# Performance work log

Measured on AMD Instinct MI355X. Metric: run time of the kernel, lower is better.

Reference implementation:

```python
import jax, jax.numpy as jnp
import numpy as np

N_NODES = 100000
N_EDGES = 1600000
G_DIM, H1, H2 = 128, 64, 32
HEADS = 4
NUM_REL = 3
NUM_CLASSES = 7


def setup_inputs() -> dict:
    key = jax.random.key(0)
    ks = jax.random.split(key, 16)
    s = 0.05
    inp = {
        "x": jax.random.normal(ks[0], (N_NODES, G_DIM), dtype=jnp.float32),
        "lengths": N_NODES,
        "edge_index": jax.random.randint(ks[1], (2, N_EDGES), 0, N_NODES),
        "edge_type": jax.random.randint(ks[2], (N_EDGES,), 0, NUM_REL),
        # RGCNConv params (root weight + per-relation weights + bias)
        "W_rel": jax.random.normal(ks[3], (NUM_REL, G_DIM, H1), dtype=jnp.float32) * s,
        "W_root": jax.random.normal(ks[4], (G_DIM, H1), dtype=jnp.float32) * s,
        "b_rgcn": jax.random.normal(ks[5], (H1,), dtype=jnp.float32) * s,
        # TransformerConv params (heads*H2 = 128 output, concat=True default)
        "Wq": jax.random.normal(ks[6], (H1, HEADS * H2), dtype=jnp.float32) * s,
        "bq": jax.random.normal(ks[7], (HEADS * H2,), dtype=jnp.float32) * s,
        "Wk": jax.random.normal(ks[8], (H1, HEADS * H2), dtype=jnp.float32) * s,
        "bk": jax.random.normal(ks[9], (HEADS * H2,), dtype=jnp.float32) * s,
        "Wv": jax.random.normal(ks[10], (H1, HEADS * H2), dtype=jnp.float32) * s,
        "bv": jax.random.normal(ks[11], (HEADS * H2,), dtype=jnp.float32) * s,
        "Wskip": jax.random.normal(ks[12], (H1, HEADS * H2), dtype=jnp.float32) * s,
        "bskip": jax.random.normal(ks[13], (HEADS * H2,), dtype=jnp.float32) * s,
        # final classifier (in = heads*H2 since TransformerConv concat=True)
        "Wf": jax.random.normal(ks[14], (HEADS * H2, NUM_CLASSES), dtype=jnp.float32) * s,
        "bf": jax.random.normal(ks[15], (NUM_CLASSES,), dtype=jnp.float32) * s,
    }
    return inp


def _forward(x, edge_index, edge_type, W_rel, W_root, b_rgcn,
             Wq, bq, Wk, bk, Wv, bv, Wskip, bskip, Wf, bf):
    n = x.shape[0]
    src, dst = edge_index[0], edge_index[1]  # source -> target flow

    # ---- RGCNConv: root transform + per-relation mean aggregation ----
    h = x @ W_root + b_rgcn  # [N, H1]
    for r in range(NUM_REL):
        hr = x @ W_rel[r]  # [N, H1] transform at node level (cheap)
        mask = (edge_type == r)
        msg = jnp.where(mask[:, None], hr[src], 0.0)  # [E, H1]
        ssum = jax.ops.segment_sum(msg, dst, num_segments=n)
        cnt = jax.ops.segment_sum(mask.astype(x.dtype), dst, num_segments=n)
        h = h + jnp.where(cnt[:, None] > 0, ssum / jnp.maximum(cnt, 1.0)[:, None], 0.0)
    h = jax.nn.relu(h)

    # ---- TransformerConv (heads=4, concat=True, root skip) ----
    Q = (h @ Wq + bq).reshape(n, HEADS, H2)
    K = (h @ Wk + bk).reshape(n, HEADS, H2)
    V = (h @ Wv + bv).reshape(n, HEADS, H2)
    scores = jnp.sum(Q[dst] * K[src], axis=-1) / jnp.sqrt(jnp.asarray(H2, x.dtype))  # [E, HEADS]
    smax = jax.ops.segment_max(scores, dst, num_segments=n)  # [N, HEADS]
    e = jnp.exp(scores - smax[dst])
    denom = jax.ops.segment_sum(e, dst, num_segments=n)  # [N, HEADS]
    alpha = e / jnp.maximum(denom[dst], 1e-16)  # [E, HEADS]
    agg = jax.ops.segment_sum(alpha[..., None] * V[src], dst, num_segments=n)  # [N, HEADS, H2]
    out = agg.reshape(n, HEADS * H2) + h @ Wskip + bskip
    out = jax.nn.relu(out)

    return out @ Wf + bf  # [N, NUM_CLASSES]


def reference(x, lengths, edge_index, edge_type, W_rel, W_root, b_rgcn,
              Wq, bq, Wk, bk, Wv, bv, Wskip, bskip, Wf, bf):
    # lengths is accepted but unused by the original forward
    return _forward(x, edge_index, edge_type, W_rel, W_root, b_rgcn,
                    Wq, bq, Wk, bk, Wv, bv, Wskip, bskip, Wf, bf)
```

## Files before the change

kernel.cpp:

```cpp
#include <hip/hip_runtime.h>
#include <math.h>

#define N_NODES 100000
#define N_EDGES 1600000

typedef short short8 __attribute__((ext_vector_type(8)));
typedef float f32x4 __attribute__((ext_vector_type(4)));
typedef float f32x2 __attribute__((ext_vector_type(2)));
typedef _Float16 h2 __attribute__((ext_vector_type(2)));

#define QSC 0.25503540f

static __device__ __forceinline__ float bf2f(unsigned int u16) {
    return __uint_as_float(u16 << 16);
}
static __device__ __forceinline__ unsigned short f2bf(float f) {
    unsigned u = __float_as_uint(f);
    unsigned r = u + 0x7FFF + ((u >> 16) & 1);
    return (unsigned short)(r >> 16);
}
static __device__ __forceinline__ f32x2 bfpair(unsigned u) {
    f32x2 r;
    r.x = __uint_as_float(u << 16);
    r.y = __uint_as_float(u & 0xFFFF0000u);
    return r;
}
static __device__ __forceinline__ float dot8h(const h2* q, uint4 k) {
    h2 s = q[0] * __builtin_bit_cast(h2, k.x);
    s += q[1] * __builtin_bit_cast(h2, k.y);
    s += q[2] * __builtin_bit_cast(h2, k.z);
    s += q[3] * __builtin_bit_cast(h2, k.w);
    return (float)s.x + (float)s.y;
}
static __device__ __forceinline__ void pv8h(h2* o, float w, uint4 v) {
    _Float16 wh = (_Float16)w;
    o[0] += wh * __builtin_bit_cast(h2, v.x);
    o[1] += wh * __builtin_bit_cast(h2, v.y);
    o[2] += wh * __builtin_bit_cast(h2, v.z);
    o[3] += wh * __builtin_bit_cast(h2, v.w);
}

__global__ void repack_kernel(const float* __restrict__ Wrel, const float* __restrict__ Wroot,
                              const float* __restrict__ Wq, const float* __restrict__ Wk,
                              const float* __restrict__ Wv, const float* __restrict__ Wsk,
                              const float* __restrict__ bq, const float* __restrict__ bk,
                              const float* __restrict__ bv, const float* __restrict__ bsk,
                              unsigned short* __restrict__ W1t, unsigned short* __restrict__ W2t,
                              float* __restrict__ bcat) {
    int idx = blockIdx.x * 256 + threadIdx.x;
    if (idx < 128 * 256) {
        int k = idx >> 8, c = idx & 255;
        float v;
        if (c < 192) { int r = c >> 6, cc = c & 63; v = Wrel[r * 8192 + k * 64 + cc]; }
        else v = Wroot[k * 64 + (c - 192)];
        W1t[c * 128 + k] = f2bf(v);
    }
    int i2 = idx - 128 * 256;
    if (i2 >= 0 && i2 < 64 * 512) {
        int k = i2 >> 9, c = i2 & 511;
        float v;
        if (c < 128) v = Wq[k * 128 + c];
        else if (c < 256) v = Wk[k * 128 + c - 128];
        else if (c < 384) v = Wv[k * 128 + c - 256];
        else v = Wsk[k * 128 + c - 384];
        W2t[c * 64 + k] = f2bf(v);
    }
    int i3 = idx - 128 * 256 - 64 * 512;
    if (i3 >= 0 && i3 < 512) {
        float v;
        if (i3 < 128) v = bq[i3];
        else if (i3 < 256) v = bk[i3 - 128];
        else if (i3 < 384) v = bv[i3 - 256];
        else v = bsk[i3 - 384];
        bcat[i3] = v;
    }
}

__global__ void hist_kernel(const int* __restrict__ ei, const int* __restrict__ et,
                            int* __restrict__ cntr) {
    int e = blockIdx.x * 256 + threadIdx.x;
    if (e < N_EDGES) atomicAdd(&cntr[et[e] * N_NODES + ei[N_EDGES + e]], 1);
}

__global__ void scanA_kernel(const int* __restrict__ cntr, int* __restrict__ part) {
    __shared__ int wsum[4];
    int t = threadIdx.x;
    int base = blockIdx.x * 1024 + t * 4;
    int s = 0;
    for (int i = 0; i < 4; i++) {
        int idx = base + i;
        if (idx < N_NODES) s += cntr[idx] + cntr[N_NODES + idx] + cntr[2 * N_NODES + idx];
    }
    for (int off = 1; off < 64; off <<= 1) s += __shfl_xor(s, off);
    if ((t & 63) == 0) wsum[t >> 6] = s;
    __syncthreads();
    if (t == 0) part[blockIdx.x] = wsum[0] + wsum[1] + wsum[2] + wsum[3];
}

__global__ void scanC_kernel(const int* __restrict__ cntr, const int* __restrict__ part,
                             int* __restrict__ rs) {
    __shared__ int wsum[4];
    __shared__ int ws2[4];
    int t = threadIdx.x;
    int lane = t & 63;
    int base = blockIdx.x * 1024 + t * 4;
    int v[4]; int tsum = 0;
    for (int i = 0; i < 4; i++) {
        int idx = base + i;
        v[i] = (idx < N_NODES) ? (cntr[idx] + cntr[N_NODES + idx] + cntr[2 * N_NODES + idx]) : 0;
        tsum += v[i];
    }
    int p = (t < blockIdx.x) ? part[t] : 0;
    for (int off = 1; off < 64; off <<= 1) p += __shfl_xor(p, off);
    if (lane == 0) ws2[t >> 6] = p;
    int x = tsum;
    for (int off = 1; off < 64; off <<= 1) { int y = __shfl_up(x, off); if (lane >= off) x += y; }
    if (lane == 63) wsum[t >> 6] = x;
    __syncthreads();
    if (t == 0) { int run = 0; for (int w = 0; w < 4; w++) { int tmp = wsum[w]; wsum[w] = run; run += tmp; } }
    __syncthreads();
    int bofs = ws2[0] + ws2[1] + ws2[2] + ws2[3];
    int excl = x - tsum + wsum[t >> 6] + bofs;
    for (int i = 0; i < 4; i++) {
        int idx = base + i;
        if (idx < N_NODES) rs[idx] = excl;
        excl += v[i];
    }
    if (blockIdx.x == 0 && t == 0) rs[N_NODES] = N_EDGES;
}

__global__ void scatter_kernel(const int* __restrict__ ei, const int* __restrict__ et,
                               const int* __restrict__ rs, const int* __restrict__ cntr,
                               int* __restrict__ fill,
                               unsigned int* __restrict__ ep, float* __restrict__ epw) {
    int e = blockIdx.x * 256 + threadIdx.x;
    if (e >= N_EDGES) return;
    int src = ei[e], dst = ei[N_EDGES + e], r = et[e];
    int pos = rs[dst] + atomicAdd(&fill[dst], 1);
    int c = cntr[r * N_NODES + dst];
    ep[pos] = ((unsigned)src << 2) | (unsigned)r;
    epw[pos] = 1.f / (float)c;
}

__global__ __launch_bounds__(256) void gemm1_mfma(const float* __restrict__ X,
                                                  const unsigned short* __restrict__ W1t,
                                                  unsigned short* __restrict__ hr_all) {
    __shared__ unsigned short As[64][136];
    __shared__ unsigned short Bs[64][136];
    int t = threadIdx.x;
    int rb = blockIdx.x * 64;
    #pragma unroll
    for (int i = 0; i < 8; i++) {
        int lin = t + i * 256;
        int row = lin >> 5;
        int c4 = lin & 31;
        float4 v = make_float4(0.f, 0.f, 0.f, 0.f);
        int gr = rb + row;
        if (gr < N_NODES) v = *(const float4*)&X[gr * 128 + c4 * 4];
        unsigned w0 = (unsigned)f2bf(v.x) | ((unsigned)f2bf(v.y) << 16);
        unsigned w1 = (unsigned)f2bf(v.z) | ((unsigned)f2bf(v.w) << 16);
        *(uint2*)&As[row][c4 * 4] = make_uint2(w0, w1);
    }
    int w = t >> 6, l = t & 63;
    int wr = (w >> 1) * 32, wc = (w & 1) * 32;
    int lr = l & 15, lk = (l >> 4) * 8;
    int drow = (l >> 4) * 4;
    int dcol = l & 15;
    for (int cb4 = 0; cb4 < 4; cb4++) {
        int cb = cb4 * 64;
        __syncthreads();
        #pragma unroll
        for (int i = 0; i < 4; i++) {
            int lin = t + i * 256;
            int n = lin >> 4;
            int k8 = lin & 15;
            *(uint4*)&Bs[n][k8 * 8] = *(const uint4*)&W1t[(cb + n) * 128 + k8 * 8];
        }
        __syncthreads();
        f32x4 c00 = {0.f,0.f,0.f,0.f}, c01 = {0.f,0.f,0.f,0.f};
        f32x4 c10 = {0.f,0.f,0.f,0.f}, c11 = {0.f,0.f,0.f,0.f};
        #pragma unroll
        for (int kk = 0; kk < 128; kk += 32) {
            short8 a0 = *(const short8*)&As[wr + lr][kk + lk];
            short8 a1 = *(const short8*)&As[wr + 16 + lr][kk + lk];
            short8 b0 = *(const short8*)&Bs[wc + lr][kk + lk];
            short8 b1 = *(const short8*)&Bs[wc + 16 + lr][kk + lk];
            c00 = __builtin_amdgcn_mfma_f32_16x16x32_bf16(a0, b0, c00, 0, 0, 0);
            c01 = __builtin_amdgcn_mfma_f32_16x16x32_bf16(a0, b1, c01, 0, 0, 0);
            c10 = __builtin_amdgcn_mfma_f32_16x16x32_bf16(a1, b0, c10, 0, 0, 0);
            c11 = __builtin_amdgcn_mfma_f32_16x16x32_bf16(a1, b1, c11, 0, 0, 0);
        }
        f32x4 cc[2][2] = {{c00, c01}, {c10, c11}};
        #pragma unroll
        for (int i = 0; i < 2; i++)
            #pragma unroll
            for (int j = 0; j < 2; j++)
                #pragma unroll
                for (int rg = 0; rg < 4; rg++) {
                    int gr = rb + wr + i * 16 + drow + rg;
                    int gc = cb + wc + j * 16 + dcol;
                    if (gr < N_NODES) hr_all[gr * 256 + gc] = f2bf(cc[i][j][rg]);
                }
    }
}

__global__ __launch_bounds__(256) void rgcn_kernel(const unsigned short* __restrict__ hr,
                                                   const float* __restrict__ brg, const int* __restrict__ rs,
                                                   const unsigned int* __restrict__ ep,
                                                   const float* __restrict__ epw,
                                                   unsigned short* __restrict__ Hm) {
    int t = threadIdx.x, lane = t & 63;
    int n = blockIdx.x * 4 + (t >> 6);
    if (n >= N_NODES) return;
    int slot = lane >> 4, pos = lane & 15;
    const uint2* H2 = (const uint2*)hr;
    f32x2 a01 = {0.f, 0.f}, a23 = {0.f, 0.f};
    int p0 = rs[n], p1 = rs[n + 1];
    for (int base = p0; base < p1; base += 64) {
        int pc = base + lane;
        unsigned chunk = (pc < p1) ? ep[pc] : 0u;
        float wch = (pc < p1) ? epw[pc] : 0.f;
        int cnt = min(64, p1 - base);
        int g0 = 0;
        for (; g0 + 16 <= cnt; g0 += 16) {
            int i0 = g0 + slot;
            int e0 = __shfl((int)chunk, i0);
            int e1 = __shfl((int)chunk, i0 + 4);
            int e2 = __shfl((int)chunk, i0 + 8);
            int e3 = __shfl((int)chunk, i0 + 12);
            float w0 = __shfl(wch, i0);
            float w1 = __shfl(wch, i0 + 4);
            float w2 = __shfl(wch, i0 + 8);
            float w3 = __shfl(wch, i0 + 12);
            uint2 h0 = H2[e0 * 16 + pos];
            uint2 h1 = H2[e1 * 16 + pos];
            uint2 h2v = H2[e2 * 16 + pos];
            uint2 h3 = H2[e3 * 16 + pos];
            a01 += w0 * bfpair(h0.x); a23 += w0 * bfpair(h0.y);
            a01 += w1 * bfpair(h1.x); a23 += w1 * bfpair(h1.y);
            a01 += w2 * bfpair(h2v.x); a23 += w2 * bfpair(h2v.y);
            a01 += w3 * bfpair(h3.x); a23 += w3 * bfpair(h3.y);
        }
        for (; g0 < cnt; g0 += 8) {
            int iA = g0 + slot, iB = iA + 4;
            int e0 = __shfl((int)chunk, iA);
            int e1 = __shfl((int)chunk, iB);
            float w0 = __shfl(wch, iA);
            float w1 = __shfl(wch, iB);
            uint2 h0 = H2[e0 * 16 + pos];
            uint2 h1 = H2[e1 * 16 + pos];
            a01 += w0 * bfpair(h0.x); a23 += w0 * bfpair(h0.y);
            a01 += w1 * bfpair(h1.x); a23 += w1 * bfpair(h1.y);
        }
    }
    a01.x += __shfl_xor(a01.x, 16); a01.x += __shfl_xor(a01.x, 32);
    a01.y += __shfl_xor(a01.y, 16); a01.y += __shfl_xor(a01.y, 32);
    a23.x += __shfl_xor(a23.x, 16); a23.x += __shfl_xor(a23.x, 32);
    a23.y += __shfl_xor(a23.y, 16); a23.y += __shfl_xor(a23.y, 32);
    uint2 rt = H2[(n * 4 + 3) * 16 + pos];
    f32x2 r01 = bfpair(rt.x), r23 = bfpair(rt.y);
    float4 bb = ((const float4*)brg)[pos];
    float h0 = fmaxf(r01.x + bb.x + a01.x, 0.f);
    float h1 = fmaxf(r01.y + bb.y + a01.y, 0.f);
    float h2s = fmaxf(r23.x + bb.z + a23.x, 0.f);
    float h3 = fmaxf(r23.y + bb.w + a23.y, 0.f);
    if (slot == 0) {
        uint2 wv;
        wv.x = (unsigned)f2bf(h0) | ((unsigned)f2bf(h1) << 16);
        wv.y = (unsigned)f2bf(h2s) | ((unsigned)f2bf(h3) << 16);
        ((uint2*)Hm)[n * 16 + pos] = wv;
    }
}

__global__ __launch_bounds__(256) void gemm2_mfma(const unsigned short* __restrict__ Hm,
                                                  const unsigned short* __restrict__ W2t,
                                                  const float* __restrict__ bcat,
                                                  _Float16* __restrict__ QS, _Float16* __restrict__ KV) {
    __shared__ unsigned short As[64][72];
    __shared__ unsigned short Bs[64][72];
    int t = threadIdx.x;
    int rb = blockIdx.x * 64;
    #pragma unroll
    for (int i = 0; i < 2; i++) {
        int lin = t + i * 256;
        int row = lin >> 3;
        int k8 = lin & 7;
        uint4 v = make_uint4(0, 0, 0, 0);
        int gr = rb + row;
        if (gr < N_NODES) v = *(const uint4*)&Hm[gr * 64 + k8 * 8];
        *(uint4*)&As[row][k8 * 8] = v;
    }
    int w = t >> 6, l = t & 63;
    int wr = (w >> 1) * 32, wc = (w & 1) * 32;
    int lr = l & 15, lk = (l >> 4) * 8;
    int drow = (l >> 4) * 4;
    int dcol = l & 15;
    for (int cb8 = 0; cb8 < 8; cb8++) {
        int cb = cb8 * 64;
        float qsc = (cb8 < 2) ? QSC : 1.f;
        __syncthreads();
        #pragma unroll
        for (int i = 0; i < 2; i++) {
            int lin = t + i * 256;
            int n = lin >> 3;
            int k8 = lin & 7;
            *(uint4*)&Bs[n][k8 * 8] = *(const uint4*)&W2t[(cb + n) * 64 + k8 * 8];
        }
        __syncthreads();
        f32x4 c00 = {0.f,0.f,0.f,0.f}, c01 = {0.f,0.f,0.f,0.f};
        f32x4 c10 = {0.f,0.f,0.f,0.f}, c11 = {0.f,0.f,0.f,0.f};
        #pragma unroll
        for (int kk = 0; kk < 64; kk += 32) {
            short8 a0 = *(const short8*)&As[wr + lr][kk + lk];
            short8 a1 = *(const short8*)&As[wr + 16 + lr][kk + lk];
            short8 b0 = *(const short8*)&Bs[wc + lr][kk + lk];
            short8 b1 = *(const short8*)&Bs[wc + 16 + lr][kk + lk];
            c00 = __builtin_amdgcn_mfma_f32_16x16x32_bf16(a0, b0, c00, 0, 0, 0);
            c01 = __builtin_amdgcn_mfma_f32_16x16x32_bf16(a0, b1, c01, 0, 0, 0);
            c10 = __builtin_amdgcn_mfma_f32_16x16x32_bf16(a1, b0, c10, 0, 0, 0);
            c11 = __builtin_amdgcn_mfma_f32_16x16x32_bf16(a1, b1, c11, 0, 0, 0);
        }
        f32x4 cc[2][2] = {{c00, c01}, {c10, c11}};
        #pragma unroll
        for (int i = 0; i < 2; i++)
            #pragma unroll
            for (int j = 0; j < 2; j++)
                #pragma unroll
                for (int rg = 0; rg < 4; rg++) {
                    int gr = rb + wr + i * 16 + drow + rg;
                    int gc = cb + wc + j * 16 + dcol;
                    if (gr >= N_NODES) continue;
                    float v = (cc[i][j][rg] + bcat[gc]) * qsc;
                    _Float16 h = (_Float16)v;
                    if (gc < 128) QS[gr * 256 + gc] = h;
                    else if (gc < 384) KV[gr * 256 + gc - 128] = h;
                    else QS[gr * 256 + gc - 256] = h;
                }
    }
}

__global__ __launch_bounds__(256) void attn_kernel(const _Float16* __restrict__ QS,
                                                   const _Float16* __restrict__ KV,
                                                   const int* __restrict__ rs, const unsigned int* __restrict__ ep,
                                                   const float* __restrict__ Wf, const float* __restrict__ bfv,
                                                   float* __restrict__ out) {
    int t = threadIdx.x, lane = t & 63;
    int n = blockIdx.x * 4 + (t >> 6);
    if (n >= N_NODES) return;
    int slot = lane >> 4, pos = lane & 15;
    const uint4* KV4 = (const uint4*)KV;
    const uint4* QS4 = (const uint4*)QS;
    uint4 qv = QS4[n * 32 + pos];
    h2 qh[4] = { __builtin_bit_cast(h2, qv.x), __builtin_bit_cast(h2, qv.y),
                 __builtin_bit_cast(h2, qv.z), __builtin_bit_cast(h2, qv.w) };
    h2 o[4] = { h2{0,0}, h2{0,0}, h2{0,0}, h2{0,0} };
    float d = 0.f;
    int p0 = rs[n], p1 = rs[n + 1];
    for (int base = p0; base < p1; base += 64) {
        int pc = base + lane;
        unsigned chunk = (pc < p1) ? ep[pc] : 0u;
        int cnt = min(64, p1 - base);
        int g0 = 0;
        for (; g0 + 16 <= cnt; g0 += 16) {
            int i0 = g0 + slot;
            int e0 = __shfl((int)chunk, i0);
            int e1 = __shfl((int)chunk, i0 + 4);
            int e2 = __shfl((int)chunk, i0 + 8);
            int e3 = __shfl((int)chunk, i0 + 12);
            int b0 = ((e0 >> 2) << 5) + pos;
            int b1 = ((e1 >> 2) << 5) + pos;
            int b2 = ((e2 >> 2) << 5) + pos;
            int b3 = ((e3 >> 2) << 5) + pos;
            uint4 k0 = KV4[b0], v0 = KV4[b0 + 16];
            uint4 k1 = KV4[b1], v1 = KV4[b1 + 16];
            uint4 k2 = KV4[b2], v2 = KV4[b2 + 16];
            uint4 k3 = KV4[b3], v3 = KV4[b3 + 16];
            float d0 = dot8h(qh, k0);
            float d1 = dot8h(qh, k1);
            float d2 = dot8h(qh, k2);
            float d3 = dot8h(qh, k3);
            d0 += __shfl_xor(d0, 1); d1 += __shfl_xor(d1, 1); d2 += __shfl_xor(d2, 1); d3 += __shfl_xor(d3, 1);
            d0 += __shfl_xor(d0, 2); d1 += __shfl_xor(d1, 2); d2 += __shfl_xor(d2, 2); d3 += __shfl_xor(d3, 2);
            float w0 = __builtin_amdgcn_exp2f(d0);
            float w1 = __builtin_amdgcn_exp2f(d1);
            float w2 = __builtin_amdgcn_exp2f(d2);
            float w3 = __builtin_amdgcn_exp2f(d3);
            d += (w0 + w1) + (w2 + w3);
            pv8h(o, w0, v0); pv8h(o, w1, v1); pv8h(o, w2, v2); pv8h(o, w3, v3);
        }
        for (; g0 < cnt; g0 += 8) {
            int iA = g0 + slot, iB = iA + 4;
            int e0 = __shfl((int)chunk, iA);
            int e1 = __shfl((int)chunk, iB);
            int b0 = ((e0 >> 2) << 5) + pos;
            int b1 = ((e1 >> 2) << 5) + pos;
            uint4 k0 = KV4[b0], v0 = KV4[b0 + 16];
            uint4 k1 = KV4[b1], v1 = KV4[b1 + 16];
            float d0 = dot8h(qh, k0);
            float d1 = dot8h(qh, k1);
            d0 += __shfl_xor(d0, 1); d1 += __shfl_xor(d1, 1);
            d0 += __shfl_xor(d0, 2); d1 += __shfl_xor(d1, 2);
            float w0 = (iA < cnt) ? __builtin_amdgcn_exp2f(d0) : 0.f;
            float w1 = (iB < cnt) ? __builtin_amdgcn_exp2f(d1) : 0.f;
            d += w0 + w1;
            pv8h(o, w0, v0); pv8h(o, w1, v1);
        }
    }
    float of[8];
    #pragma unroll
    for (int i = 0; i < 4; i++) { of[2 * i] = (float)o[i].x; of[2 * i + 1] = (float)o[i].y; }
    d += __shfl_xor(d, 16); d += __shfl_xor(d, 32);
    #pragma unroll
    for (int i = 0; i < 8; i++) { of[i] += __shfl_xor(of[i], 16); of[i] += __shfl_xor(of[i], 32); }
    float inv = (d > 0.f) ? 1.f / d : 0.f;
    uint4 sv = QS4[n * 32 + 16 + pos];
    h2 sh[4] = { __builtin_bit_cast(h2, sv.x), __builtin_bit_cast(h2, sv.y),
                 __builtin_bit_cast(h2, sv.z), __builtin_bit_cast(h2, sv.w) };
    float rf[8];
    #pragma unroll
    for (int i = 0; i < 4; i++) {
        rf[2 * i]     = fmaxf((float)sh[i].x + of[2 * i] * inv, 0.f);
        rf[2 * i + 1] = fmaxf((float)sh[i].y + of[2 * i + 1] * inv, 0.f);
    }
    float rr0 = (slot == 0) ? rf[0] : (slot == 1) ? rf[2] : (slot == 2) ? rf[4] : rf[6];
    float rr1 = (slot == 0) ? rf[1] : (slot == 1) ? rf[3] : (slot == 2) ? rf[5] : rf[7];
    int gd = pos * 8 + slot * 2;
    float acc[7];
    #pragma unroll
    for (int j = 0; j < 7; j++) acc[j] = rr0 * Wf[gd * 7 + j] + rr1 * Wf[gd * 7 + 7 + j];
    #pragma unroll
    for (int j = 0; j < 7; j++) {
        acc[j] += __shfl_xor(acc[j], 1);
        acc[j] += __shfl_xor(acc[j], 2);
        acc[j] += __shfl_xor(acc[j], 4);
        acc[j] += __shfl_xor(acc[j], 8);
        acc[j] += __shfl_xor(acc[j], 16);
        acc[j] += __shfl_xor(acc[j], 32);
    }
    if (lane == 0) {
        #pragma unroll
        for (int j = 0; j < 7; j++) out[n * 7 + j] = acc[j] + bfv[j];
    }
}

extern "C" void kernel_launch(void* const* d_in, const int* in_sizes, int n_in,
                              void* d_out, int out_size, void* d_ws, size_t ws_size,
                              hipStream_t stream) {
    const float* x     = (const float*)d_in[0];
    const int*   ei    = (const int*)d_in[2];
    const int*   et    = (const int*)d_in[3];
    const float* Wrel  = (const float*)d_in[4];
    const float* Wroot = (const float*)d_in[5];
    const float* brg   = (const float*)d_in[6];
    const float* Wq    = (const float*)d_in[7];
    const float* bq    = (const float*)d_in[8];
    const float* Wk    = (const float*)d_in[9];
    const float* bk    = (const float*)d_in[10];
    const float* Wv    = (const float*)d_in[11];
    const float* bv    = (const float*)d_in[12];
    const float* Wsk   = (const float*)d_in[13];
    const float* bsk   = (const float*)d_in[14];
    const float* Wf    = (const float*)d_in[15];
    const float* bfv   = (const float*)d_in[16];
    float* out = (float*)d_out;

    char* ws = (char*)d_ws;
    unsigned short* hr_all = (unsigned short*)(ws + 0);
    _Float16*       QS     = (_Float16*)(ws + 0);
    _Float16*       KV     = (_Float16*)(ws + 51200000);
    unsigned short* Hm     = (unsigned short*)(ws + 102400000);
    unsigned int*   ep     = (unsigned int*)(ws + 115200000);
    float*          epw    = (float*)(ws + 121600000);
    int*            rs     = (int*)(ws + 128000000);
    int*            cntr   = (int*)(ws + 128400016);
    int*            fill   = (int*)(ws + 129600016);
    int*            part   = (int*)(ws + 130000016);
    unsigned short* W1t    = (unsigned short*)(ws + 130000528);
    unsigned short* W2t    = (unsigned short*)(ws + 130066064);
    float*          bcat   = (float*)(ws + 130131600);

    hipMemsetAsync(cntr, 0, 4 * N_NODES * sizeof(int), stream);

    repack_kernel<<<258, 256, 0, stream>>>(Wrel, Wroot, Wq, Wk, Wv, Wsk, bq, bk, bv, bsk, W1t, W2t, bcat);

    hist_kernel<<<N_EDGES / 256, 256, 0, stream>>>(ei, et, cntr);
    scanA_kernel<<<98, 256, 0, stream>>>(cntr, part);
    scanC_kernel<<<98, 256, 0, stream>>>(cntr, part, rs);
    scatter_kernel<<<N_EDGES / 256, 256, 0, stream>>>(ei, et, rs, cntr, fill, ep, epw);

    gemm1_mfma<<<1563, 256, 0, stream>>>(x, W1t, hr_all);
    rgcn_kernel<<<25000, 256, 0, stream>>>(hr_all, brg, rs, ep, epw, Hm);

    gemm2_mfma<<<1563, 256, 0, stream>>>(Hm, W2t, bcat, QS, KV);
    attn_kernel<<<25000, 256, 0, stream>>>(QS, KV, rs, ep, Wf, bfv, out);
}
```

Measured before the change: 504.5 us.

## Sort edges by destination and relation using histogram ranks, drop per-edge weights

The histogram atomic's return value is stored as a per-edge rank, and the scan emits per-node relation sub-offsets (uint4). Scatter then places each edge without a second atomic pass or a fill array. The per-edge weight array is removed, and rgcn computes 1/count per relation from the offsets. This cuts atomics, one memset region and an edge-sized float read and write. In exchange it writes and reads an extra rank array, and edges become grouped by relation within each node.

Measured after the change: 440.1 us. -12.8%, faster.

```diff
diff --git a/kernel.cpp b/kernel.cpp
--- a/kernel.cpp
+++ b/kernel.cpp
@@ -77,9 +77,9 @@
 }
 
 __global__ void hist_kernel(const int* __restrict__ ei, const int* __restrict__ et,
-                            int* __restrict__ cntr) {
+                            int* __restrict__ cntr, int* __restrict__ rank) {
     int e = blockIdx.x * 256 + threadIdx.x;
-    if (e < N_EDGES) atomicAdd(&cntr[et[e] * N_NODES + ei[N_EDGES + e]], 1);
+    if (e < N_EDGES) rank[e] = atomicAdd(&cntr[et[e] * N_NODES + ei[N_EDGES + e]], 1);
 }
 
 __global__ void scanA_kernel(const int* __restrict__ cntr, int* __restrict__ part) {
@@ -98,17 +98,19 @@
 }
 
 __global__ void scanC_kernel(const int* __restrict__ cntr, const int* __restrict__ part,
-                             int* __restrict__ rs) {
+                             uint4* __restrict__ bro) {
     __shared__ int wsum[4];
     __shared__ int ws2[4];
     int t = threadIdx.x;
     int lane = t & 63;
     int base = blockIdx.x * 1024 + t * 4;
-    int v[4]; int tsum = 0;
+    int c0v[4], c1v[4], c2v[4]; int tsum = 0;
     for (int i = 0; i < 4; i++) {
         int idx = base + i;
-        v[i] = (idx < N_NODES) ? (cntr[idx] + cntr[N_NODES + idx] + cntr[2 * N_NODES + idx]) : 0;
-        tsum += v[i];
+        if (idx < N_NODES) {
+            c0v[i] = cntr[idx]; c1v[i] = cntr[N_NODES + idx]; c2v[i] = cntr[2 * N_NODES + idx];
+        } else { c0v[i] = c1v[i] = c2v[i] = 0; }
+        tsum += c0v[i] + c1v[i] + c2v[i];
     }
     int p = (t < blockIdx.x) ? part[t] : 0;
     for (int off = 1; off < 64; off <<= 1) p += __shfl_xor(p, off);
@@ -123,23 +125,27 @@
     int excl = x - tsum + wsum[t >> 6] + bofs;
     for (int i = 0; i < 4; i++) {
         int idx = base + i;
-        if (idx < N_NODES) rs[idx] = excl;
-        excl += v[i];
-    }
-    if (blockIdx.x == 0 && t == 0) rs[N_NODES] = N_EDGES;
+        if (idx < N_NODES) {
+            uint4 b;
+            b.x = (unsigned)excl;
+            b.y = (unsigned)(excl + c0v[i]);
+            b.z = (unsigned)(excl + c0v[i] + c1v[i]);
+            b.w = (unsigned)(excl + c0v[i] + c1v[i] + c2v[i]);
+            bro[idx] = b;
+        }
+        excl += c0v[i] + c1v[i] + c2v[i];
+    }
 }
 
 __global__ void scatter_kernel(const int* __restrict__ ei, const int* __restrict__ et,
-                               const int* __restrict__ rs, const int* __restrict__ cntr,
-                               int* __restrict__ fill,
-                               unsigned int* __restrict__ ep, float* __restrict__ epw) {
+                               const uint4* __restrict__ bro, const int* __restrict__ rank,
+                               unsigned int* __restrict__ ep) {
     int e = blockIdx.x * 256 + threadIdx.x;
     if (e >= N_EDGES) return;
-    int src = ei[e], dst = ei[N_EDGES + e], r = et[e];
-    int pos = rs[dst] + atomicAdd(&fill[dst], 1);
-    int c = cntr[r * N_NODES + dst];
-    ep[pos] = ((unsigned)src << 2) | (unsigned)r;
-    epw[pos] = 1.f / (float)c;
+    int src = ei[e], dst = ei[N_EDGES + e], r = et[e], rk = rank[e];
+    uint4 b = bro[dst];
+    unsigned ofs = (r == 0) ? b.x : (r == 1) ? b.y : b.z;
+    ep[ofs + rk] = ((unsigned)src << 2) | (unsigned)r;
 }
 
 __global__ __launch_bounds__(256) void gemm1_mfma(const float* __restrict__ X,
@@ -205,37 +211,41 @@
 }
 
 __global__ __launch_bounds__(256) void rgcn_kernel(const unsigned short* __restrict__ hr,
-                                                   const float* __restrict__ brg, const int* __restrict__ rs,
+                                                   const float* __restrict__ brg,
+                                                   const uint4* __restrict__ bro,
                                                    const unsigned int* __restrict__ ep,
-                                                   const float* __restrict__ epw,
                                                    unsigned short* __restrict__ Hm) {
     int t = threadIdx.x, lane = t & 63;
     int n = blockIdx.x * 4 + (t >> 6);
     if (n >= N_NODES) return;
     int slot = lane >> 4, pos = lane & 15;
     const uint2* H2 = (const uint2*)hr;
+    uint4 b = bro[n];
+    int p0 = (int)b.x, p1 = (int)b.w;
+    int c0 = (int)(b.y - b.x), c1 = (int)(b.z - b.y), c2 = (int)(b.w - b.z);
+    float i0 = c0 ? 1.f / (float)c0 : 0.f;
+    float i1 = c1 ? 1.f / (float)c1 : 0.f;
+    float i2 = c2 ? 1.f / (float)c2 : 0.f;
     f32x2 a01 = {0.f, 0.f}, a23 = {0.f, 0.f};
-    int p0 = rs[n], p1 = rs[n + 1];
     for (int base = p0; base < p1; base += 64) {
         int pc = base + lane;
         unsigned chunk = (pc < p1) ? ep[pc] : 0u;
-        float wch = (pc < p1) ? epw[pc] : 0.f;
         int cnt = min(64, p1 - base);
         int g0 = 0;
         for (; g0 + 16 <= cnt; g0 += 16) {
-            int i0 = g0 + slot;
-            int e0 = __shfl((int)chunk, i0);
-            int e1 = __shfl((int)chunk, i0 + 4);
-            int e2 = __shfl((int)chunk, i0 + 8);
-            int e3 = __shfl((int)chunk, i0 + 12);
-            float w0 = __shfl(wch, i0);
-            float w1 = __shfl(wch, i0 + 4);
-            float w2 = __shfl(wch, i0 + 8);
-            float w3 = __shfl(wch, i0 + 12);
-            uint2 h0 = H2[e0 * 16 + pos];
-            uint2 h1 = H2[e1 * 16 + pos];
-            uint2 h2v = H2[e2 * 16 + pos];
-            uint2 h3 = H2[e3 * 16 + pos];
+            int i0x = g0 + slot;
+            int e0 = __shfl((int)chunk, i0x);
+            int e1 = __shfl((int)chunk, i0x + 4);
+            int e2 = __shfl((int)chunk, i0x + 8);
+            int e3 = __shfl((int)chunk, i0x + 12);
+            float w0 = ((e0 & 3) == 0) ? i0 : ((e0 & 3) == 1) ? i1 : i2;
+            float w1 = ((e1 & 3) == 0) ? i0 : ((e1 & 3) == 1) ? i1 : i2;
+            float w2 = ((e2 & 3) == 0) ? i0 : ((e2 & 3) == 1) ? i1 : i2;
+            float w3 = ((e3 & 3) == 0) ? i0 : ((e3 & 3) == 1) ? i1 : i2;
+            uint2 h0 = H2[(unsigned)e0 * 16 + pos];
+            uint2 h1 = H2[(unsigned)e1 * 16 + pos];
+            uint2 h2v = H2[(unsigned)e2 * 16 + pos];
+            uint2 h3 = H2[(unsigned)e3 * 16 + pos];
             a01 += w0 * bfpair(h0.x); a23 += w0 * bfpair(h0.y);
             a01 += w1 * bfpair(h1.x); a23 += w1 * bfpair(h1.y);
             a01 += w2 * bfpair(h2v.x); a23 += w2 * bfpair(h2v.y);
@@ -245,10 +255,12 @@
             int iA = g0 + slot, iB = iA + 4;
             int e0 = __shfl((int)chunk, iA);
             int e1 = __shfl((int)chunk, iB);
-            float w0 = __shfl(wch, iA);
-            float w1 = __shfl(wch, iB);
-            uint2 h0 = H2[e0 * 16 + pos];
-            uint2 h1 = H2[e1 * 16 + pos];
+            float w0 = ((e0 & 3) == 0) ? i0 : ((e0 & 3) == 1) ? i1 : i2;
+            float w1 = ((e1 & 3) == 0) ? i0 : ((e1 & 3) == 1) ? i1 : i2;
+            w0 = (iA < cnt) ? w0 : 0.f;
+            w1 = (iB < cnt) ? w1 : 0.f;
+            uint2 h0 = H2[(unsigned)e0 * 16 + pos];
+            uint2 h1 = H2[(unsigned)e1 * 16 + pos];
             a01 += w0 * bfpair(h0.x); a23 += w0 * bfpair(h0.y);
             a01 += w1 * bfpair(h1.x); a23 += w1 * bfpair(h1.y);
         }
@@ -341,7 +353,8 @@
 
 __global__ __launch_bounds__(256) void attn_kernel(const _Float16* __restrict__ QS,
                                                    const _Float16* __restrict__ KV,
-                                                   const int* __restrict__ rs, const unsigned int* __restrict__ ep,
+                                                   const uint4* __restrict__ bro,
+                                                   const unsigned int* __restrict__ ep,
                                                    const float* __restrict__ Wf, const float* __restrict__ bfv,
                                                    float* __restrict__ out) {
     int t = threadIdx.x, lane = t & 63;
@@ -355,7 +368,8 @@
                  __builtin_bit_cast(h2, qv.z), __builtin_bit_cast(h2, qv.w) };
     h2 o[4] = { h2{0,0}, h2{0,0}, h2{0,0}, h2{0,0} };
     float d = 0.f;
-    int p0 = rs[n], p1 = rs[n + 1];
+    uint4 bnd = bro[n];
+    int p0 = (int)bnd.x, p1 = (int)bnd.w;
     for (int base = p0; base < p1; base += 64) {
         int pc = base + lane;
         unsigned chunk = (pc < p1) ? ep[pc] : 0u;
@@ -470,27 +484,26 @@
     _Float16*       KV     = (_Float16*)(ws + 51200000);
     unsigned short* Hm     = (unsigned short*)(ws + 102400000);
     unsigned int*   ep     = (unsigned int*)(ws + 115200000);
-    float*          epw    = (float*)(ws + 121600000);
-    int*            rs     = (int*)(ws + 128000000);
-    int*            cntr   = (int*)(ws + 128400016);
-    int*            fill   = (int*)(ws + 129600016);
-    int*            part   = (int*)(ws + 130000016);
-    unsigned short* W1t    = (unsigned short*)(ws + 130000528);
-    unsigned short* W2t    = (unsigned short*)(ws + 130066064);
-    float*          bcat   = (float*)(ws + 130131600);
-
-    hipMemsetAsync(cntr, 0, 4 * N_NODES * sizeof(int), stream);
+    int*            rank   = (int*)(ws + 121600000);
+    uint4*          bro    = (uint4*)(ws + 128000000);
+    int*            cntr   = (int*)(ws + 129600016);
+    int*            part   = (int*)(ws + 130800016);
+    unsigned short* W1t    = (unsigned short*)(ws + 130800528);
+    unsigned short* W2t    = (unsigned short*)(ws + 130866064);
+    float*          bcat   = (float*)(ws + 130931600);
+
+    hipMemsetAsync(cntr, 0, 3 * N_NODES * sizeof(int), stream);
 
     repack_kernel<<<258, 256, 0, stream>>>(Wrel, Wroot, Wq, Wk, Wv, Wsk, bq, bk, bv, bsk, W1t, W2t, bcat);
 
-    hist_kernel<<<N_EDGES / 256, 256, 0, stream>>>(ei, et, cntr);
+    hist_kernel<<<N_EDGES / 256, 256, 0, stream>>>(ei, et, cntr, rank);
     scanA_kernel<<<98, 256, 0, stream>>>(cntr, part);
-    scanC_kernel<<<98, 256, 0, stream>>>(cntr, part, rs);
-    scatter_kernel<<<N_EDGES / 256, 256, 0, stream>>>(ei, et, rs, cntr, fill, ep, epw);
+    scanC_kernel<<<98, 256, 0, stream>>>(cntr, part, bro);
+    scatter_kernel<<<N_EDGES / 256, 256, 0, stream>>>(ei, et, bro, rank, ep);
 
     gemm1_mfma<<<1563, 256, 0, stream>>>(x, W1t, hr_all);
-    rgcn_kernel<<<25000, 256, 0, stream>>>(hr_all, brg, rs, ep, epw, Hm);
+    rgcn_kernel<<<25000, 256, 0, stream>>>(hr_all, brg, bro, ep, Hm);
 
     gemm2_mfma<<<1563, 256, 0, stream>>>(Hm, W2t, bcat, QS, KV);
-    attn_kernel<<<25000, 256, 0, stream>>>(QS, KV, rs, ep, Wf, bfv, out);
-}
+    attn_kernel<<<25000, 256, 0, stream>>>(QS, KV, bro, ep, Wf, bfv, out);
+}
```
